# Kernel tuning notes

Hardware: AMD Instinct MI355X
Metric: run time of the kernel (lower is better)

## Reference

```python
import jax, jax.numpy as jnp
import numpy as np

# Constants from __init__ (domain bounds)
X_MIN, X_MAX = -1.0, 1.0
Y_MIN, Y_MAX = -1.0, 1.0
T_MIN, T_MAX = 0.0, 1.0

N_POINTS = 262144
WIDTH = 128
N_HIDDEN_STACK = 5  # hidden->hidden layers between first and last


def setup_inputs() -> dict:
    key = jax.random.key(0)
    ks = jax.random.split(key, 8)
    X = jax.random.uniform(ks[0], (N_POINTS, 4), dtype=jnp.float32)
    # glorot_normal-ish init
    def glorot(k, fan_in, fan_out, shape):
        std = (2.0 / (fan_in + fan_out)) ** 0.5
        return jax.random.normal(k, shape, dtype=jnp.float32) * std
    W0 = glorot(ks[1], 4, WIDTH, (4, WIDTH))
    b0 = jnp.zeros((WIDTH,), dtype=jnp.float32)
    Wh = glorot(ks[2], WIDTH, WIDTH, (N_HIDDEN_STACK, WIDTH, WIDTH))
    bh = jnp.zeros((N_HIDDEN_STACK, WIDTH), dtype=jnp.float32)
    WL = glorot(ks[3], WIDTH, 2, (WIDTH, 2))
    bL = jnp.zeros((2,), dtype=jnp.float32)
    nu_min = jnp.zeros((), dtype=jnp.float32)
    nu_max = jnp.ones((), dtype=jnp.float32)
    return {"X": X, "nu_min": nu_min, "nu_max": nu_max,
            "W0": W0, "b0": b0, "Wh": Wh, "bh": bh, "WL": WL, "bL": bL}


def _swish(x):
    return x * jax.nn.sigmoid(x)


def reference(X, nu_min, nu_max, W0, b0, Wh, bh, WL, bL):
    # Input rescaling to [-1, 1] per feature, then concat
    x_s = 2.0 * (X[:, 0:1] - X_MIN) / (X_MAX - X_MIN) - 1.0
    y_s = 2.0 * (X[:, 1:2] - Y_MIN) / (Y_MAX - Y_MIN) - 1.0
    t_s = 2.0 * (X[:, 2:3] - T_MIN) / (T_MAX - T_MIN) - 1.0
    nu_s = 2.0 * (X[:, 3:4] - nu_min) / (nu_max - nu_min) - 1.0
    H = jnp.concatenate([x_s, y_s, t_s, nu_s], axis=1)  # [N, 4]
    # Stacked small dense + swish layers (fused-MLP candidate)
    H = _swish(H @ W0 + b0)  # [N, WIDTH]
    for i in range(Wh.shape[0]):
        H = _swish(H @ Wh[i] + bh[i])
    return H @ WL + bL  # [N, 2], no activation on output layer
```

## Files before the change

kernel.cpp:

```cpp
#include <hip/hip_runtime.h>

typedef __bf16 bf16x8 __attribute__((ext_vector_type(8)));
typedef __bf16 bf16x2 __attribute__((ext_vector_type(2)));
typedef float  f32x4  __attribute__((ext_vector_type(4)));

#define WS_WT0_B 0
#define WS_WTH_B 8192
#define WS_WLT_B 172032

__device__ __forceinline__ unsigned short f2b(float f) {
  return __builtin_bit_cast(unsigned short, (__bf16)f);
}

__global__ void prep_kernel(const float* __restrict__ W0,
                            const float* __restrict__ Wh,
                            const float* __restrict__ WL,
                            unsigned short* __restrict__ ws) {
  int i = blockIdx.x * 256 + threadIdx.x;
  int l  = (i >> 3) & 63;
  int j  = i & 7;
  int lm = l & 15, lh = l >> 4;
  if (i < 4096) {
    int nt = i >> 9;
    int n = nt * 16 + lm, k = lh * 8 + j;
    ws[i] = f2b(k < 4 ? W0[k * 128 + n] : 0.f);
  } else if (i < 86016) {
    int t = i - 4096;
    int frag = t >> 9;
    int nt = frag & 7, ks = (frag >> 3) & 3, h = frag >> 5;
    int n = nt * 16 + lm, k = ks * 32 + lh * 8 + j;
    ws[i] = f2b(Wh[(h * 128 + k) * 128 + n]);
  } else if (i < 90112) {
    int t = i - 86016;
    int f = t >> 9;
    int k = (f & 3) * 32 + lh * 8 + j;
    ws[i] = f2b((f < 4 && lm < 2) ? WL[k * 2 + lm] : 0.f);
  }
}

__device__ __forceinline__ f32x4 swish4(f32x4 z) {
  const f32x4 u = z * (-1.44269504088896340736f);
  f32x4 e;
#if __has_builtin(__builtin_amdgcn_exp2f)
  e[0] = __builtin_amdgcn_exp2f(u[0]); e[1] = __builtin_amdgcn_exp2f(u[1]);
  e[2] = __builtin_amdgcn_exp2f(u[2]); e[3] = __builtin_amdgcn_exp2f(u[3]);
#else
  e[0] = __expf(u[0] * 0.6931471805599453f); e[1] = __expf(u[1] * 0.6931471805599453f);
  e[2] = __expf(u[2] * 0.6931471805599453f); e[3] = __expf(u[3] * 0.6931471805599453f);
#endif
  const f32x4 w = e + 1.f;
  f32x4 s;
  s[0] = __builtin_amdgcn_rcpf(w[0]); s[1] = __builtin_amdgcn_rcpf(w[1]);
  s[2] = __builtin_amdgcn_rcpf(w[2]); s[3] = __builtin_amdgcn_rcpf(w[3]);
  return z * s;
}

__device__ __forceinline__ uint2 pack4(f32x4 r) {
  bf16x2 lo = {(__bf16)r[0], (__bf16)r[1]};
  bf16x2 hi = {(__bf16)r[2], (__bf16)r[3]};
  uint2 wv;
  wv.x = __builtin_bit_cast(unsigned int, lo);
  wv.y = __builtin_bit_cast(unsigned int, hi);
  return wv;
}

#define LRD(addr) __builtin_bit_cast(bf16x8, *reinterpret_cast<const uint4*>(addr))
#define MFMA(a, b, c) __builtin_amdgcn_mfma_f32_16x16x32_bf16((a), (b), (c), 0, 0, 0)

__device__ __forceinline__ void stage8k(const char* src, char* dst, int tid) {
  const int woff = (tid >> 6) * 1024;
#if __has_builtin(__builtin_amdgcn_global_load_lds)
  __builtin_amdgcn_global_load_lds(
      (const __attribute__((address_space(1))) unsigned int*)(src + tid * 16),
      (__attribute__((address_space(3))) unsigned int*)(dst + woff), 16, 0, 0);
  __builtin_amdgcn_global_load_lds(
      (const __attribute__((address_space(1))) unsigned int*)(src + 4096 + tid * 16),
      (__attribute__((address_space(3))) unsigned int*)(dst + 4096 + woff), 16, 0, 0);
#else
  const uint4 v0 = *reinterpret_cast<const uint4*>(src + tid * 16);
  const uint4 v1 = *reinterpret_cast<const uint4*>(src + 4096 + tid * 16);
  *reinterpret_cast<uint4*>(dst + tid * 16) = v0;
  *reinterpret_cast<uint4*>(dst + 4096 + tid * 16) = v1;
#endif
}

__launch_bounds__(256, 4)
__global__ void mlp_kernel(const float* __restrict__ X,
                           const float* __restrict__ nu_min_p,
                           const float* __restrict__ nu_max_p,
                           const float* __restrict__ b0,
                           const float* __restrict__ bh,
                           const float* __restrict__ bL,
                           const unsigned short* __restrict__ ws,
                           float* __restrict__ out) {
  __shared__ __align__(16) char smem[16384 + 16384 + 2560];
  char* Hs  = smem;
  char* wb0 = smem + 16384;
  char* wb1 = smem + 24576;
  float* bias_lds = reinterpret_cast<float*>(smem + 32768);
  const int tid  = threadIdx.x;
  const int lane = tid & 63, wave = tid >> 6;
  const int lm = lane & 15, lh = lane >> 4;
  const int row0 = blockIdx.x * 64;
  const char* wsb = reinterpret_cast<const char*>(ws);
  const int xorm = (lm & 7) << 4;
  const int ntb = wave * 2;
  int vaG[4], waG[4];
#pragma unroll
  for (int g = 0; g < 4; ++g) {
    vaG[g] = (g * 16 + lm) * 256 + ((lh * 16) ^ xorm);
    waG[g] = (g * 16 + lm) * 256 + (((lh * 8) ^ xorm) ^ (wave << 6));
  }

  stage8k(wsb + WS_WT0_B, wb1, tid);
#pragma unroll
  for (int i = 0; i < 3; ++i) {
    const int idx = i * 256 + tid;
    if (idx < 640) bias_lds[idx] = bh[idx];
  }
  if (tid < 64) {
    const float4 xv = reinterpret_cast<const float4*>(X)[row0 + tid];
    const float numin = nu_min_p[0], numax = nu_max_p[0];
    const float v0 = xv.x;
    const float v1 = xv.y;
    const float v2 = 2.f * xv.z - 1.f;
    const float v3 = 2.f * (xv.w - numin) / (numax - numin) - 1.f;
    uint4 c0;
    c0.x = (unsigned)f2b(v0) | ((unsigned)f2b(v1) << 16);
    c0.y = (unsigned)f2b(v2) | ((unsigned)f2b(v3) << 16);
    c0.z = 0u; c0.w = 0u;
    const uint4 z4 = make_uint4(0u, 0u, 0u, 0u);
    const int xr = (tid & 7) << 4;
    char* rp = Hs + tid * 256;
    *reinterpret_cast<uint4*>(rp + (0  ^ xr)) = c0;
    *reinterpret_cast<uint4*>(rp + (16 ^ xr)) = z4;
    *reinterpret_cast<uint4*>(rp + (32 ^ xr)) = z4;
    *reinterpret_cast<uint4*>(rp + (48 ^ xr)) = z4;
  }
  __syncthreads();

  f32x4 acc[2][4];
  bf16x8 a0, a1;

  {
    stage8k(wsb + WS_WTH_B, wb0, tid);
    a0 = LRD(wb1 + (ntb + 0) * 1024 + lane * 16);
    a1 = LRD(wb1 + (ntb + 1) * 1024 + lane * 16);
    const f32x4 bv0 = *reinterpret_cast<const f32x4*>(b0 + (ntb + 0) * 16 + lh * 4);
    const f32x4 bv1 = *reinterpret_cast<const f32x4*>(b0 + (ntb + 1) * 16 + lh * 4);
#pragma unroll
    for (int g = 0; g < 4; ++g) {
      const bf16x8 f = LRD(Hs + vaG[g]);
      acc[0][g] = MFMA(a0, f, bv0);
      acc[1][g] = MFMA(a1, f, bv1);
    }
    __syncthreads();
#pragma unroll
    for (int j = 0; j < 2; ++j)
#pragma unroll
      for (int g = 0; g < 4; ++g) {
        const uint2 wv = pack4(swish4(acc[j][g]));
        *reinterpret_cast<uint2*>(Hs + (waG[g] ^ (j << 5))) = wv;
      }
    __syncthreads();
  }

#define HPHASE(RBUF, SBUF, SRC, KSOFF, C0, C1)                               \
  do {                                                                       \
    stage8k((SRC), (SBUF), tid);                                             \
    a0 = LRD((RBUF) + (ntb + 0) * 1024 + lane * 16);                         \
    a1 = LRD((RBUF) + (ntb + 1) * 1024 + lane * 16);                         \
    _Pragma("unroll")                                                        \
    for (int g = 0; g < 4; ++g) {                                            \
      const bf16x8 f = LRD(Hs + (vaG[g] ^ (KSOFF)));                         \
      acc[0][g] = MFMA(a0, f, (C0));                                         \
      acc[1][g] = MFMA(a1, f, (C1));                                         \
    }                                                                        \
  } while (0)

#pragma unroll 1
  for (int h = 0; h < 5; ++h) {
    const char* wsrc = wsb + WS_WTH_B + h * 32768;
    const char* nsrc = (h < 4) ? (wsrc + 32768) : (wsb + WS_WLT_B);
    const f32x4 bv0 = *reinterpret_cast<const f32x4*>(bias_lds + h * 128 + (ntb + 0) * 16 + lh * 4);
    const f32x4 bv1 = *reinterpret_cast<const f32x4*>(bias_lds + h * 128 + (ntb + 1) * 16 + lh * 4);

    HPHASE(wb0, wb1, wsrc + 8192,  0,   bv0, bv1);
    __syncthreads();
    HPHASE(wb1, wb0, wsrc + 16384, 64,  acc[0][g], acc[1][g]);
    __syncthreads();
    HPHASE(wb0, wb1, wsrc + 24576, 128, acc[0][g], acc[1][g]);
    __syncthreads();
    HPHASE(wb1, wb0, nsrc,         192, acc[0][g], acc[1][g]);
    __syncthreads();
#pragma unroll
    for (int j = 0; j < 2; ++j)
#pragma unroll
      for (int g = 0; g < 4; ++g) {
        const uint2 wv = pack4(swish4(acc[j][g]));
        *reinterpret_cast<uint2*>(Hs + (waG[g] ^ (j << 5))) = wv;
      }
    __syncthreads();
  }
#undef HPHASE

  {
    const float bl0 = bL[0], bl1 = bL[1];
    const int vaF = (wave * 16 + lm) * 256 + ((lh * 16) ^ xorm);
    f32x4 accL = {0.f, 0.f, 0.f, 0.f};
#pragma unroll
    for (int ks = 0; ks < 4; ++ks) {
      const bf16x8 a = LRD(wb0 + ks * 1024 + lane * 16);
      const bf16x8 f = LRD(Hs + (vaF ^ (ks << 6)));
      accL = MFMA(a, f, accL);
    }
    if (lh == 0) {
      const int p = wave * 16 + lm;
      float2 o;
      o.x = accL[0] + bl0;
      o.y = accL[1] + bl1;
      *reinterpret_cast<float2*>(out + (size_t)(row0 + p) * 2) = o;
    }
  }
}

extern "C" void kernel_launch(void* const* d_in, const int* in_sizes, int n_in,
                              void* d_out, int out_size, void* d_ws, size_t ws_size,
                              hipStream_t stream) {
  const float* X     = (const float*)d_in[0];
  const float* numin = (const float*)d_in[1];
  const float* numax = (const float*)d_in[2];
  const float* W0    = (const float*)d_in[3];
  const float* b0    = (const float*)d_in[4];
  const float* Wh    = (const float*)d_in[5];
  const float* bh    = (const float*)d_in[6];
  const float* WL    = (const float*)d_in[7];
  const float* bL    = (const float*)d_in[8];
  unsigned short* ws = (unsigned short*)d_ws;
  float* out = (float*)d_out;

  hipLaunchKernelGGL(prep_kernel, dim3(352), dim3(256), 0, stream, W0, Wh, WL, ws);
  hipLaunchKernelGGL(mlp_kernel, dim3(4096), dim3(256), 0, stream,
                     X, numin, numax, b0, bh, bL, ws, out);
}
```

Baseline: 78.77 us.

## Deepen weight staging to four LDS buffers with partial vmcnt waits

Weight slices are staged through four 8 KB LDS buffers instead of two, so the global-to-LDS copy for a slice is issued three phases ahead of its use. The full __syncthreads between phases is replaced by s_waitcnt vmcnt(4) plus a raw s_barrier, which lets recent copies stay in flight. The goal is to hide global load latency behind the MFMA work. In exchange LDS use grows from about 34 KB to 50 KB per block and launch bounds drop to 3 blocks per CU, which lowers occupancy; the hand-written waitcnt counts must also match the number of outstanding loads exactly.

```diff
diff --git a/kernel.cpp b/kernel.cpp
--- a/kernel.cpp
+++ b/kernel.cpp
@@ -66,6 +66,10 @@
 
 #define LRD(addr) __builtin_bit_cast(bf16x8, *reinterpret_cast<const uint4*>(addr))
 #define MFMA(a, b, c) __builtin_amdgcn_mfma_f32_16x16x32_bf16((a), (b), (c), 0, 0, 0)
+#define SB() __builtin_amdgcn_sched_barrier(0)
+#define WAITVM(N) asm volatile("s_waitcnt vmcnt(" #N ")" ::: "memory")
+#define WAITLGKM() asm volatile("s_waitcnt lgkmcnt(0)" ::: "memory")
+#define LBAR() do { SB(); __builtin_amdgcn_s_barrier(); SB(); } while (0)
 
 __device__ __forceinline__ void stage8k(const char* src, char* dst, int tid) {
   const int woff = (tid >> 6) * 1024;
@@ -84,7 +88,7 @@
 #endif
 }
 
-__launch_bounds__(256, 4)
+__launch_bounds__(256, 3)
 __global__ void mlp_kernel(const float* __restrict__ X,
                            const float* __restrict__ nu_min_p,
                            const float* __restrict__ nu_max_p,
@@ -93,11 +97,10 @@
                            const float* __restrict__ bL,
                            const unsigned short* __restrict__ ws,
                            float* __restrict__ out) {
-  __shared__ __align__(16) char smem[16384 + 16384 + 2560];
+  __shared__ __align__(16) char smem[16384 + 4 * 8192 + 2560];
   char* Hs  = smem;
-  char* wb0 = smem + 16384;
-  char* wb1 = smem + 24576;
-  float* bias_lds = reinterpret_cast<float*>(smem + 32768);
+  char* wb[4] = { smem + 16384, smem + 24576, smem + 32768, smem + 40960 };
+  float* bias_lds = reinterpret_cast<float*>(smem + 49152);
   const int tid  = threadIdx.x;
   const int lane = tid & 63, wave = tid >> 6;
   const int lm = lane & 15, lh = lane >> 4;
@@ -112,7 +115,6 @@
     waG[g] = (g * 16 + lm) * 256 + (((lh * 8) ^ xorm) ^ (wave << 6));
   }
 
-  stage8k(wsb + WS_WT0_B, wb1, tid);
 #pragma unroll
   for (int i = 0; i < 3; ++i) {
     const int idx = i * 256 + tid;
@@ -137,15 +139,18 @@
     *reinterpret_cast<uint4*>(rp + (32 ^ xr)) = z4;
     *reinterpret_cast<uint4*>(rp + (48 ^ xr)) = z4;
   }
+  stage8k(wsb + WS_WT0_B, wb[0], tid);
+  stage8k(wsb + WS_WTH_B, wb[1], tid);
+  stage8k(wsb + WS_WTH_B + 8192, wb[2], tid);
   __syncthreads();
 
   f32x4 acc[2][4];
   bf16x8 a0, a1;
 
   {
-    stage8k(wsb + WS_WTH_B, wb0, tid);
-    a0 = LRD(wb1 + (ntb + 0) * 1024 + lane * 16);
-    a1 = LRD(wb1 + (ntb + 1) * 1024 + lane * 16);
+    stage8k(wsb + WS_WTH_B + 16384, wb[3], tid);
+    a0 = LRD(wb[0] + (ntb + 0) * 1024 + lane * 16);
+    a1 = LRD(wb[0] + (ntb + 1) * 1024 + lane * 16);
     const f32x4 bv0 = *reinterpret_cast<const f32x4*>(b0 + (ntb + 0) * 16 + lh * 4);
     const f32x4 bv1 = *reinterpret_cast<const f32x4*>(b0 + (ntb + 1) * 16 + lh * 4);
 #pragma unroll
@@ -154,7 +159,7 @@
       acc[0][g] = MFMA(a0, f, bv0);
       acc[1][g] = MFMA(a1, f, bv1);
     }
-    __syncthreads();
+    WAITLGKM(); LBAR();
 #pragma unroll
     for (int j = 0; j < 2; ++j)
 #pragma unroll
@@ -162,14 +167,14 @@
         const uint2 wv = pack4(swish4(acc[j][g]));
         *reinterpret_cast<uint2*>(Hs + (waG[g] ^ (j << 5))) = wv;
       }
-    __syncthreads();
-  }
-
-#define HPHASE(RBUF, SBUF, SRC, KSOFF, C0, C1)                               \
+    WAITLGKM(); LBAR();
+  }
+
+#define HPHASE(RBI, SBI, SRC, KSOFF, C0, C1)                                 \
   do {                                                                       \
-    stage8k((SRC), (SBUF), tid);                                             \
-    a0 = LRD((RBUF) + (ntb + 0) * 1024 + lane * 16);                         \
-    a1 = LRD((RBUF) + (ntb + 1) * 1024 + lane * 16);                         \
+    stage8k((SRC), wb[SBI], tid);                                            \
+    a0 = LRD(wb[RBI] + (ntb + 0) * 1024 + lane * 16);                        \
+    a1 = LRD(wb[RBI] + (ntb + 1) * 1024 + lane * 16);                        \
     _Pragma("unroll")                                                        \
     for (int g = 0; g < 4; ++g) {                                            \
       const bf16x8 f = LRD(Hs + (vaG[g] ^ (KSOFF)));                         \
@@ -181,18 +186,21 @@
 #pragma unroll 1
   for (int h = 0; h < 5; ++h) {
     const char* wsrc = wsb + WS_WTH_B + h * 32768;
-    const char* nsrc = (h < 4) ? (wsrc + 32768) : (wsb + WS_WLT_B);
+    const char* st0 = wsrc + 24576;
+    const char* st1 = (h < 4) ? (wsrc + 32768)         : (wsb + WS_WLT_B);
+    const char* st2 = (h < 4) ? (wsrc + 32768 + 8192)  : (wsb + WS_WT0_B);
+    const char* st3 = (h < 4) ? (wsrc + 32768 + 16384) : (wsb + WS_WT0_B);
     const f32x4 bv0 = *reinterpret_cast<const f32x4*>(bias_lds + h * 128 + (ntb + 0) * 16 + lh * 4);
     const f32x4 bv1 = *reinterpret_cast<const f32x4*>(bias_lds + h * 128 + (ntb + 1) * 16 + lh * 4);
 
-    HPHASE(wb0, wb1, wsrc + 8192,  0,   bv0, bv1);
-    __syncthreads();
-    HPHASE(wb1, wb0, wsrc + 16384, 64,  acc[0][g], acc[1][g]);
-    __syncthreads();
-    HPHASE(wb0, wb1, wsrc + 24576, 128, acc[0][g], acc[1][g]);
-    __syncthreads();
-    HPHASE(wb1, wb0, nsrc,         192, acc[0][g], acc[1][g]);
-    __syncthreads();
+    HPHASE(1, 0, st0, 0,   bv0, bv1);
+    WAITVM(4); LBAR();
+    HPHASE(2, 1, st1, 64,  acc[0][g], acc[1][g]);
+    WAITVM(4); LBAR();
+    HPHASE(3, 2, st2, 128, acc[0][g], acc[1][g]);
+    WAITVM(4); LBAR();
+    HPHASE(0, 3, st3, 192, acc[0][g], acc[1][g]);
+    WAITVM(4); WAITLGKM(); LBAR();
 #pragma unroll
     for (int j = 0; j < 2; ++j)
 #pragma unroll
@@ -200,7 +208,7 @@
         const uint2 wv = pack4(swish4(acc[j][g]));
         *reinterpret_cast<uint2*>(Hs + (waG[g] ^ (j << 5))) = wv;
       }
-    __syncthreads();
+    WAITLGKM(); LBAR();
   }
 #undef HPHASE
 
@@ -210,7 +218,7 @@
     f32x4 accL = {0.f, 0.f, 0.f, 0.f};
 #pragma unroll
     for (int ks = 0; ks < 4; ++ks) {
-      const bf16x8 a = LRD(wb0 + ks * 1024 + lane * 16);
+      const bf16x8 a = LRD(wb[1] + ks * 1024 + lane * 16);
       const bf16x8 f = LRD(Hs + (vaF ^ (ks << 6)));
       accL = MFMA(a, f, accL);
     }
```

Result: slower. 81.85 us (+3.9%).
